# Kernel tuning notes

Hardware: AMD Instinct MI355X
Metric: run time of the kernel (lower is better)

Reference implementation:

```python
import jax, jax.numpy as jnp
import numpy as np

V, E, H, O, B, T = 50000, 128, 128, 128, 64, 512


def setup_inputs() -> dict:
    key = jax.random.key(0)
    ks = jax.random.split(key, 16)
    s = 0.05
    X = jax.random.randint(ks[0], (B, T), 0, V)
    lens = jnp.sort(jax.random.randint(ks[1], (B,), 64, T + 1))[::-1]
    lens = lens.at[0].set(T)  # pack_padded needs descending lengths, max == T
    emb = jax.random.normal(ks[2], (V, E)) * s
    emb = emb.at[0].set(0.0)  # padding_idx = 0
    return {
        "X": X,
        "X_lengths": lens,
        "batch_size": B,
        "emb": emb,
        "W_e2i": jax.random.normal(ks[3], (H, E)) * s,
        "b_e2i": jax.random.normal(ks[4], (H,)) * s,
        "Wih_f": jax.random.normal(ks[5], (3 * H, H)) * s,
        "Whh_f": jax.random.normal(ks[6], (3 * H, H)) * s,
        "bih_f": jax.random.normal(ks[7], (3 * H,)) * s,
        "bhh_f": jax.random.normal(ks[8], (3 * H,)) * s,
        "Wih_b": jax.random.normal(ks[9], (3 * H, H)) * s,
        "Whh_b": jax.random.normal(ks[10], (3 * H, H)) * s,
        "bih_b": jax.random.normal(ks[11], (3 * H,)) * s,
        "bhh_b": jax.random.normal(ks[12], (3 * H,)) * s,
        "W_h2o": jax.random.normal(ks[13], (O, 2 * H)) * s,
        "b_h2o": jax.random.normal(ks[14], (O,)) * s,
        "u_w": jax.random.uniform(ks[15], (O,)),  # torch.rand
    }


def _gru_scan(gx, mask_tb, Whh, bhh):
    """gx: [T,B,3H] precomputed input gates; mask_tb: [T,B,1] valid-step mask.
    Masked update emulates pack_padded_sequence: padded steps keep h unchanged
    (and h stays 0 before the first valid step of the reversed direction)."""
    h0 = jnp.zeros((gx.shape[1], Whh.shape[1]), gx.dtype)

    def step(h, tb):
        gxt, m = tb
        gh = h @ Whh.T + bhh
        gxr, gxz, gxn = jnp.split(gxt, 3, axis=-1)
        ghr, ghz, ghn = jnp.split(gh, 3, axis=-1)
        r = jax.nn.sigmoid(gxr + ghr)
        z = jax.nn.sigmoid(gxz + ghz)
        n = jnp.tanh(gxn + r * ghn)
        h_new = (1.0 - z) * n + z * h
        h = jnp.where(m, h_new, h)
        return h, h

    _, hs = jax.lax.scan(step, h0, (gx, mask_tb))
    return hs  # [T,B,H]


def reference(X, X_lengths, batch_size, emb, W_e2i, b_e2i,
              Wih_f, Whh_f, bih_f, bhh_f, Wih_b, Whh_b, bih_b, bhh_b,
              W_h2o, b_h2o, u_w):
    x = emb[X]                              # [B,T,E]
    x = x @ W_e2i.T + b_e2i                 # [B,T,H]
    Tn = x.shape[1]
    mask = jnp.arange(Tn)[None, :] < X_lengths[:, None]  # [B,T]
    m_tb = mask.T[:, :, None]               # [T,B,1]

    gx_f = (x @ Wih_f.T + bih_f).transpose(1, 0, 2)       # [T,B,3H]
    h_f = _gru_scan(gx_f, m_tb, Whh_f, bhh_f)             # [T,B,H]
    gx_b = (x @ Wih_b.T + bih_b).transpose(1, 0, 2)[::-1]
    h_b = _gru_scan(gx_b, m_tb[::-1], Whh_b, bhh_b)[::-1]

    Hout = jnp.concatenate([h_f, h_b], axis=-1).transpose(1, 0, 2)  # [B,T,2H]
    Hout = Hout * mask[:, :, None].astype(Hout.dtype)  # pad_packed zeros pads

    Y = jnp.tanh(Hout @ W_h2o.T + b_h2o)               # [B,T,O]
    scores = jnp.where(mask, (Y * u_w).sum(-1), -jnp.inf)  # [B,T]
    alpha = jax.nn.softmax(scores, axis=1)             # per-sample softmax over valid steps
    pooled = jnp.einsum("bt,btd->bd", alpha, Hout)     # [B,2H]
    return pooled[None]                                # [1,B,2H]
```

## Files before the change

### kernel.cpp

```cpp
#include <hip/hip_runtime.h>
#include <hip/hip_bf16.h>

#define VV 50000
#define EE 128
#define HH 128
#define OO 128
#define BB 64
#define TT 512

typedef __bf16 bf16_t;
typedef __attribute__((ext_vector_type(8))) __bf16 bf16x8;
typedef __attribute__((ext_vector_type(4))) __bf16 bf16x4;
typedef __attribute__((ext_vector_type(4))) float floatx4;

#define SC_RZ (-1.4426950408889634f)
#define SC_N  (2.8853900817779268f)

__device__ __forceinline__ bf16x8 ldb8(const bf16_t* p) {
    return *reinterpret_cast<const bf16x8*>(p);
}

__device__ __forceinline__ bf16x8 ldf8_bf(const float* p) {
    const float4* q = reinterpret_cast<const float4*>(p);
    float4 u = q[0], v = q[1];
    bf16x8 r;
    r[0] = (__bf16)u.x; r[1] = (__bf16)u.y; r[2] = (__bf16)u.z; r[3] = (__bf16)u.w;
    r[4] = (__bf16)v.x; r[5] = (__bf16)v.y; r[6] = (__bf16)v.z; r[7] = (__bf16)v.w;
    return r;
}

__device__ __forceinline__ float fast_rcp(float x) { return __builtin_amdgcn_rcpf(x); }
__device__ __forceinline__ float exp2_f(float x) { return __builtin_amdgcn_exp2f(x); }
__device__ __forceinline__ float tanh_f(float x) {
    float e = __expf(2.0f * x);
    return 1.0f - 2.0f * fast_rcp(e + 1.0f);
}

__device__ __forceinline__ void lds_barrier() {
    asm volatile("s_waitcnt lgkmcnt(0)\n\ts_barrier" ::: "memory");
}

__global__ __launch_bounds__(256) void k0_conv(
    const float* __restrict__ we,
    const float* __restrict__ wihf, const float* __restrict__ wihb,
    const float* __restrict__ whhf, const float* __restrict__ whhb,
    const float* __restrict__ wh2o,
    const float* __restrict__ bihf, const float* __restrict__ bhhf,
    const float* __restrict__ bihb, const float* __restrict__ bhhb,
    bf16_t* __restrict__ we_bf,
    bf16_t* __restrict__ wih_bf, bf16_t* __restrict__ whh_bf,
    bf16_t* __restrict__ wh2o_bf, float* __restrict__ gxbias) {
    int tid = blockIdx.x * 256 + threadIdx.x;
    int np = gridDim.x * 256;
    for (int i = tid; i < HH * EE; i += np) we_bf[i] = (bf16_t)we[i];
    for (int i = tid; i < 384 * HH; i += np) {
        int nrow = i >> 7;
        float sc = (nrow < 256) ? SC_RZ : SC_N;
        wih_bf[i] = (bf16_t)(sc * wihf[i]);
        wih_bf[384 * HH + i] = (bf16_t)(sc * wihb[i]);
        whh_bf[i] = (bf16_t)(sc * whhf[i]);
        whh_bf[384 * HH + i] = (bf16_t)(sc * whhb[i]);
    }
    for (int i = tid; i < OO * 256; i += np) wh2o_bf[i] = (bf16_t)wh2o[i];
    if (tid < 768) {
        int dir = tid / 384, n = tid % 384;
        const float* bih = dir ? bihb : bihf;
        const float* bhh = dir ? bhhb : bhhf;
        float sc = (n < 256) ? SC_RZ : SC_N;
        gxbias[tid] = sc * bih[n] + (n < 256 ? sc * bhh[n] : 0.0f);
    }
}

__global__ __launch_bounds__(256) void k12_gx(const int* __restrict__ X,
                                              const float* __restrict__ emb,
                                              const bf16_t* __restrict__ we_bf,
                                              const float* __restrict__ be,
                                              const bf16_t* __restrict__ wih_bf,
                                              const float* __restrict__ gxbias,
                                              const int* __restrict__ lens,
                                              bf16_t* __restrict__ gx3) {
    int blk = blockIdx.x;
    int tq = blk >> 2;
    int g = blk & 3;
    if (4 * tq >= lens[16 * g]) return;

    int lane = threadIdx.x & 63;
    int w2 = threadIdx.x >> 6;
    int quad = lane >> 4, col = lane & 15;

    __shared__ bf16_t xs[4][16 * 136];

    {
        int t = 4 * tq + w2;
        int v = X[(g * 16 + col) * TT + t];
        bf16x8 a[4];
#pragma unroll
        for (int kc = 0; kc < 4; ++kc)
            a[kc] = ldf8_bf(emb + (size_t)v * EE + kc * 32 + quad * 8);
#pragma unroll
        for (int nt = 0; nt < 8; ++nt) {
            int n = nt * 16 + col;
            floatx4 acc = {0.f, 0.f, 0.f, 0.f};
#pragma unroll
            for (int kc = 0; kc < 4; ++kc) {
                bf16x8 bw = ldb8(we_bf + (size_t)n * EE + kc * 32 + quad * 8);
                acc = __builtin_amdgcn_mfma_f32_16x16x32_bf16(a[kc], bw, acc, 0, 0, 0);
            }
            float bias = be[n];
#pragma unroll
            for (int r = 0; r < 4; ++r)
                xs[w2][(quad * 4 + r) * 136 + n] = (bf16_t)(acc[r] + bias);
        }
    }
    __syncthreads();

    bf16x8 a2[4][4];
#pragma unroll
    for (int tt = 0; tt < 4; ++tt)
#pragma unroll
        for (int kc = 0; kc < 4; ++kc)
            a2[tt][kc] = ldb8(xs[tt] + col * 136 + kc * 32 + quad * 8);

#pragma unroll 2
    for (int tl = 0; tl < 12; ++tl) {
        int idx = w2 * 12 + tl;
        int dir = idx >= 24;
        int n = (idx - dir * 24) * 16 + col;
        bf16x8 bw[4];
#pragma unroll
        for (int kc = 0; kc < 4; ++kc)
            bw[kc] = ldb8(wih_bf + ((size_t)dir * 384 + n) * HH + kc * 32 + quad * 8);
        float bias = gxbias[dir * 384 + n];
#pragma unroll
        for (int tt = 0; tt < 4; ++tt) {
            int t = 4 * tq + tt;
            floatx4 acc = {0.f, 0.f, 0.f, 0.f};
#pragma unroll
            for (int kc = 0; kc < 4; ++kc)
                acc = __builtin_amdgcn_mfma_f32_16x16x32_bf16(a2[tt][kc], bw[kc], acc, 0, 0, 0);
            bf16x4 pack;
#pragma unroll
            for (int r = 0; r < 4; ++r)
                pack[r] = (__bf16)(acc[r] + bias);
            *reinterpret_cast<bf16x4*>(
                gx3 + (((size_t)(dir * 16 + 4 * g + quad) * TT + t) * 384 + n) * 4) = pack;
        }
    }
}

#define HPAD 144
#define HBUF (4 * HPAD)
__global__ __launch_bounds__(512) void k3_gru(const bf16_t* __restrict__ gx3,
                                              const bf16_t* __restrict__ whh_bf,
                                              const float* __restrict__ bhh_f,
                                              const float* __restrict__ bhh_b,
                                              const int* __restrict__ lens,
                                              bf16_t* __restrict__ hist2) {
    int g16 = blockIdx.x;
    int dir = blockIdx.y;
    const float* bhh = dir ? bhh_b : bhh_f;

    int tid = threadIdx.x;
    int w = tid >> 6;
    int lane = tid & 63;
    int quad = lane >> 4, col = lane & 15;
    int j = 16 * w + col;

    __shared__ bf16_t hl[2 * HBUF];
    for (int i = tid; i < 2 * HBUF; i += 512) hl[i] = (bf16_t)0.f;

    int len1 = lens[4 * g16 + quad];
    int Lmax = max(max(lens[4 * g16], lens[4 * g16 + 1]),
                   max(lens[4 * g16 + 2], lens[4 * g16 + 3]));

    float bhn = SC_N * bhh[256 + j];

    bf16x8 Bw[3][4];
#pragma unroll
    for (int gate = 0; gate < 3; ++gate)
#pragma unroll
        for (int kc = 0; kc < 4; ++kc)
            Bw[gate][kc] = ldb8(whh_bf + ((size_t)dir * 384 + gate * 128 + j) * HH + kc * 32 + quad * 8);

    const bf16_t* gbase = gx3 + (size_t)(dir * 16 + g16) * TT * 1536;
    bf16_t* hb = hist2 + (size_t)(dir * 16 + g16) * TT * 512;
    int loff[3];
#pragma unroll
    for (int gate = 0; gate < 3; ++gate)
        loff[gate] = (gate * 128 + j) * 4 + quad;
    int hoff = quad * 128 + j;
    int aoff = (col >> 2) * HPAD + quad * 8;

    float h = 0.f;
    int S4 = (Lmax + 3) & ~3;

    __bf16 ring[4][3];
#pragma unroll
    for (int u = 0; u < 4; ++u) {
        int t = dir ? (Lmax - 1 - u) : u;
#pragma unroll
        for (int gate = 0; gate < 3; ++gate)
            ring[u][gate] = gbase[(size_t)t * 1536 + loff[gate]];
    }
    lds_barrier();

    int gstep = dir ? -1536 : 1536;
    int hstep = dir ? -512 : 512;
    const bf16_t* rp0 = gbase + (size_t)(dir ? (Lmax - 5) : 4) * 1536 + loff[0];
    const bf16_t* rp1 = gbase + (size_t)(dir ? (Lmax - 5) : 4) * 1536 + loff[1];
    const bf16_t* rp2 = gbase + (size_t)(dir ? (Lmax - 5) : 4) * 1536 + loff[2];
    bf16_t* hp = hb + (size_t)(dir ? (Lmax - 1) : 0) * 512 + hoff;
    int ulo = dir ? (Lmax - len1) : 0;
    int uhi = dir ? Lmax : len1;

    for (int sb = 0; sb < S4; sb += 4) {
#pragma unroll
        for (int u = 0; u < 4; ++u) {
            int s = sb + u;
            const bf16_t* hc = hl + (s & 1) * HBUF;
            bf16_t* hn = hl + ((s + 1) & 1) * HBUF;

            float gx0 = (float)ring[u][0];
            float gx1 = (float)ring[u][1];
            float gx2 = (float)ring[u][2];

            bf16x8 a[4];
#pragma unroll
            for (int kc = 0; kc < 4; ++kc)
                a[kc] = ldb8(hc + aoff + kc * 32);

            floatx4 cr = {0.f, 0.f, 0.f, 0.f};
            floatx4 cz = {0.f, 0.f, 0.f, 0.f};
            floatx4 cn = {bhn, bhn, bhn, bhn};
#pragma unroll
            for (int kc = 0; kc < 4; ++kc) {
                cr = __builtin_amdgcn_mfma_f32_16x16x32_bf16(a[kc], Bw[0][kc], cr, 0, 0, 0);
                cz = __builtin_amdgcn_mfma_f32_16x16x32_bf16(a[kc], Bw[1][kc], cz, 0, 0, 0);
                cn = __builtin_amdgcn_mfma_f32_16x16x32_bf16(a[kc], Bw[2][kc], cn, 0, 0, 0);
            }

            ring[u][0] = *rp0;
            ring[u][1] = *rp1;
            ring[u][2] = *rp2;
            {
                int adv = (s < Lmax - 5) ? gstep : 0;
                rp0 += adv; rp1 += adv; rp2 += adv;
            }

            float rg = fast_rcp(1.0f + exp2_f(cr[0] + gx0));
            float zg = fast_rcp(1.0f + exp2_f(cz[0] + gx1));
            float v  = fmaf(rg, cn[0], gx2);
            float ng = fmaf(-2.0f, fast_rcp(exp2_f(v) + 1.0f), 1.0f);
            float hnew = fmaf(zg, h - ng, ng);

            bool upd = (s >= ulo) && (s < uhi);
            h = upd ? hnew : h;
            bf16_t h16 = (bf16_t)h;
            hn[quad * HPAD + j] = h16;
            *hp = h16;
            hp += (s < Lmax - 1) ? hstep : 0;

            lds_barrier();
        }
    }
}

__global__ __launch_bounds__(512) void k45_pool(const bf16_t* __restrict__ hist2,
                                                const bf16_t* __restrict__ wh2o_bf,
                                                const float* __restrict__ bh2o,
                                                const float* __restrict__ uw,
                                                const int* __restrict__ lens,
                                                float* __restrict__ out) {
    int b = blockIdx.x;
    int g16 = b >> 2, bl = b & 3;
    int tid = threadIdx.x;
    int lane = tid & 63, wv = tid >> 6;
    int quad = lane >> 4, col = lane & 15;
    int len = lens[b];

    int p = wv >> 2;
    int q = wv & 3;

    __shared__ float smax[TT][4];
    __shared__ float alpha[TT];
    __shared__ float redw[16];
    __shared__ float red2[16 * 32 * 9];

    const bf16_t* hf = hist2 + (size_t)g16 * TT * 512 + bl * 128;
    const bf16_t* hbk = hist2 + (size_t)(16 + g16) * TT * 512 + bl * 128;

    int n0 = (q * 2 + 0) * 16 + col;
    int n1 = (q * 2 + 1) * 16 + col;
    float bias0 = bh2o[n0], u0 = uw[n0];
    float bias1 = bh2o[n1], u1 = uw[n1];

    bf16x8 bw0[8], bw1[8];
#pragma unroll
    for (int kc = 0; kc < 8; ++kc) {
        bw0[kc] = ldb8(wh2o_bf + (size_t)n0 * 256 + kc * 32 + quad * 8);
        bw1[kc] = ldb8(wh2o_bf + (size_t)n1 * 256 + kc * 32 + quad * 8);
    }

    int nch = (len + 15) >> 4;
    bf16x8 a[8], an[8];
    {
        int t = p * 16 + col;
#pragma unroll
        for (int kc = 0; kc < 4; ++kc) {
            a[kc]     = ldb8(hf  + (size_t)t * 512 + kc * 32 + quad * 8);
            a[kc + 4] = ldb8(hbk + (size_t)t * 512 + kc * 32 + quad * 8);
        }
    }
    for (int ch = p; ch < nch; ch += 2) {
        int t0 = ch * 16;
        {
            int tn = (ch + 2 < nch ? t0 + 32 : t0) + col;
#pragma unroll
            for (int kc = 0; kc < 4; ++kc) {
                an[kc]     = ldb8(hf  + (size_t)tn * 512 + kc * 32 + quad * 8);
                an[kc + 4] = ldb8(hbk + (size_t)tn * 512 + kc * 32 + quad * 8);
            }
        }
        float p4[4] = {0.f, 0.f, 0.f, 0.f};
#pragma unroll
        for (int tl = 0; tl < 2; ++tl) {
            float bias = tl ? bias1 : bias0;
            float u = tl ? u1 : u0;
            floatx4 accA = {0.f, 0.f, 0.f, 0.f};
            floatx4 accB = {0.f, 0.f, 0.f, 0.f};
#pragma unroll
            for (int kc = 0; kc < 4; ++kc) {
                bf16x8 bwA = tl ? bw1[kc] : bw0[kc];
                bf16x8 bwB = tl ? bw1[kc + 4] : bw0[kc + 4];
                accA = __builtin_amdgcn_mfma_f32_16x16x32_bf16(a[kc], bwA, accA, 0, 0, 0);
                accB = __builtin_amdgcn_mfma_f32_16x16x32_bf16(a[kc + 4], bwB, accB, 0, 0, 0);
            }
#pragma unroll
            for (int r = 0; r < 4; ++r)
                p4[r] += tanh_f(accA[r] + accB[r] + bias) * u;
        }
#pragma unroll
        for (int m = 1; m < 16; m <<= 1)
#pragma unroll
            for (int r = 0; r < 4; ++r)
                p4[r] += __shfl_xor(p4[r], m, 64);
        if (col == 0) {
#pragma unroll
            for (int r = 0; r < 4; ++r)
                smax[t0 + quad * 4 + r][q] = p4[r];
        }
#pragma unroll
        for (int kc = 0; kc < 8; ++kc) a[kc] = an[kc];
    }
    __syncthreads();

    int t = tid;
    float s = -1e30f;
    if (t < len) s = smax[t][0] + smax[t][1] + smax[t][2] + smax[t][3];
    float m = s;
#pragma unroll
    for (int off = 1; off <= 32; off <<= 1) m = fmaxf(m, __shfl_xor(m, off, 64));
    if (lane == 0) redw[wv] = m;
    __syncthreads();
    float mx = fmaxf(fmaxf(fmaxf(redw[0], redw[1]), fmaxf(redw[2], redw[3])),
                     fmaxf(fmaxf(redw[4], redw[5]), fmaxf(redw[6], redw[7])));
    float e = (t < len) ? __expf(s - mx) : 0.f;
    alpha[t] = e;
    float sm = e;
#pragma unroll
    for (int off = 1; off <= 32; off <<= 1) sm += __shfl_xor(sm, off, 64);
    if (lane == 0) redw[8 + wv] = sm;
    __syncthreads();
    float inv = fast_rcp(redw[8] + redw[9] + redw[10] + redw[11] +
                         redw[12] + redw[13] + redw[14] + redw[15]);

    {
        int ts = tid >> 5, o = tid & 31;
        int dirp = o >> 4;
        int j8 = (o & 15) * 8;
        const bf16_t* hbase = (dirp ? hbk : hf) + j8;
        float acc8[8];
#pragma unroll
        for (int ee = 0; ee < 8; ++ee) acc8[ee] = 0.f;
        for (int tt2 = ts; tt2 < len; tt2 += 16) {
            float al = alpha[tt2];
            bf16x8 hv = ldb8(hbase + (size_t)tt2 * 512);
#pragma unroll
            for (int ee = 0; ee < 8; ++ee) acc8[ee] = fmaf(al, (float)hv[ee], acc8[ee]);
        }
#pragma unroll
        for (int ee = 0; ee < 8; ++ee) red2[(ts * 32 + o) * 9 + ee] = acc8[ee];
        __syncthreads();
        if (tid < 256) {
            int c = tid;
            int dir2 = c >> 7, rem = c & 127;
            int oo = dir2 * 16 + (rem >> 3), ee = c & 7;
            float acc = 0.f;
#pragma unroll
            for (int qq = 0; qq < 16; ++qq) acc += red2[(qq * 32 + oo) * 9 + ee];
            out[(size_t)b * 256 + c] = acc * inv;
        }
    }
}

extern "C" void kernel_launch(void* const* d_in, const int* in_sizes, int n_in,
                              void* d_out, int out_size, void* d_ws, size_t ws_size,
                              hipStream_t stream) {
    const int* X       = (const int*)d_in[0];
    const int* lens    = (const int*)d_in[1];
    const float* emb   = (const float*)d_in[3];
    const float* We2i  = (const float*)d_in[4];
    const float* be2i  = (const float*)d_in[5];
    const float* Wihf  = (const float*)d_in[6];
    const float* Whhf  = (const float*)d_in[7];
    const float* bihf  = (const float*)d_in[8];
    const float* bhhf  = (const float*)d_in[9];
    const float* Wihb  = (const float*)d_in[10];
    const float* Whhb  = (const float*)d_in[11];
    const float* bihb  = (const float*)d_in[12];
    const float* bhhb  = (const float*)d_in[13];
    const float* Wh2o  = (const float*)d_in[14];
    const float* bh2o  = (const float*)d_in[15];
    const float* uw    = (const float*)d_in[16];

    char* ws = (char*)d_ws;
    size_t off = 0;
    bf16_t* we_bf = (bf16_t*)(ws + off);   off += (size_t)HH * EE * 2;
    bf16_t* wih_bf = (bf16_t*)(ws + off);  off += (size_t)2 * 384 * HH * 2;
    bf16_t* whh_bf = (bf16_t*)(ws + off);  off += (size_t)2 * 384 * HH * 2;
    bf16_t* wh2o_bf = (bf16_t*)(ws + off); off += (size_t)OO * 256 * 2;
    float* gxbias = (float*)(ws + off);    off += 768 * 4;
    off = (off + 255) & ~(size_t)255;
    bf16_t* gx3 = (bf16_t*)(ws + off);     off += (size_t)32 * TT * 384 * 4 * 2;
    bf16_t* hist2 = (bf16_t*)(ws + off);   off += (size_t)32 * TT * 4 * 128 * 2;

    float* out = (float*)d_out;

    k0_conv<<<dim3(256), dim3(256), 0, stream>>>(We2i, Wihf, Wihb, Whhf, Whhb,
                                                 Wh2o, bihf, bhhf, bihb, bhhb,
                                                 we_bf, wih_bf, whh_bf, wh2o_bf, gxbias);
    k12_gx<<<dim3(TT), dim3(256), 0, stream>>>(X, emb, we_bf, be2i, wih_bf, gxbias, lens, gx3);
    k3_gru<<<dim3(16, 2), dim3(512), 0, stream>>>(gx3, whh_bf, bhhf, bhhb, lens, hist2);
    k45_pool<<<dim3(BB), dim3(512), 0, stream>>>(hist2, wh2o_bf, bh2o, uw, lens, out);
}
```

Baseline: 341.7 us.

## Split score and pooling kernels to spread attention scoring over more blocks

Splits the fused score/pool kernel in two. The scoring MFMA work is now spread across four blocks per sample (256 blocks instead of 64), and partial scores go to a global workspace. A second kernel per sample reads the scores, runs the softmax and does the weighted pooling. This raises parallelism on the GPU's many CUs, at the cost of an extra launch and a global round trip for the scores.

```diff
diff --git a/kernel.cpp b/kernel.cpp
--- a/kernel.cpp
+++ b/kernel.cpp
@@ -265,13 +265,14 @@
     }
 }
 
-__global__ __launch_bounds__(512) void k45_pool(const bf16_t* __restrict__ hist2,
+__global__ __launch_bounds__(512) void k4_score(const bf16_t* __restrict__ hist2,
                                                 const bf16_t* __restrict__ wh2o_bf,
                                                 const float* __restrict__ bh2o,
                                                 const float* __restrict__ uw,
                                                 const int* __restrict__ lens,
-                                                float* __restrict__ out) {
-    int b = blockIdx.x;
+                                                float* __restrict__ smax_ws) {
+    int blk = blockIdx.x;
+    int b = blk >> 2, seg = blk & 3;
     int g16 = b >> 2, bl = b & 3;
     int tid = threadIdx.x;
     int lane = tid & 63, wv = tid >> 6;
@@ -280,14 +281,12 @@
 
     int p = wv >> 2;
     int q = wv & 3;
-
-    __shared__ float smax[TT][4];
-    __shared__ float alpha[TT];
-    __shared__ float redw[16];
-    __shared__ float red2[16 * 32 * 9];
+    int ch0 = seg * 2 + p;
+    int nch = (len + 15) >> 4;
 
     const bf16_t* hf = hist2 + (size_t)g16 * TT * 512 + bl * 128;
     const bf16_t* hbk = hist2 + (size_t)(16 + g16) * TT * 512 + bl * 128;
+    float* sm = smax_ws + (size_t)b * TT * 4;
 
     int n0 = (q * 2 + 0) * 16 + col;
     int n1 = (q * 2 + 1) * 16 + col;
@@ -301,20 +300,19 @@
         bw1[kc] = ldb8(wh2o_bf + (size_t)n1 * 256 + kc * 32 + quad * 8);
     }
 
-    int nch = (len + 15) >> 4;
     bf16x8 a[8], an[8];
     {
-        int t = p * 16 + col;
+        int t = ch0 * 16 + col;
 #pragma unroll
         for (int kc = 0; kc < 4; ++kc) {
             a[kc]     = ldb8(hf  + (size_t)t * 512 + kc * 32 + quad * 8);
             a[kc + 4] = ldb8(hbk + (size_t)t * 512 + kc * 32 + quad * 8);
         }
     }
-    for (int ch = p; ch < nch; ch += 2) {
+    for (int ch = ch0; ch < nch; ch += 8) {
         int t0 = ch * 16;
         {
-            int tn = (ch + 2 < nch ? t0 + 32 : t0) + col;
+            int tn = (ch + 8 < nch ? t0 + 128 : t0) + col;
 #pragma unroll
             for (int kc = 0; kc < 4; ++kc) {
                 an[kc]     = ldb8(hf  + (size_t)tn * 512 + kc * 32 + quad * 8);
@@ -347,16 +345,37 @@
         if (col == 0) {
 #pragma unroll
             for (int r = 0; r < 4; ++r)
-                smax[t0 + quad * 4 + r][q] = p4[r];
+                sm[(size_t)(t0 + quad * 4 + r) * 4 + q] = p4[r];
         }
 #pragma unroll
         for (int kc = 0; kc < 8; ++kc) a[kc] = an[kc];
     }
-    __syncthreads();
+}
+
+__global__ __launch_bounds__(512) void k5_pool(const bf16_t* __restrict__ hist2,
+                                               const float* __restrict__ smax_ws,
+                                               const int* __restrict__ lens,
+                                               float* __restrict__ out) {
+    int b = blockIdx.x;
+    int g16 = b >> 2, bl = b & 3;
+    int tid = threadIdx.x;
+    int lane = tid & 63, wv = tid >> 6;
+    int len = lens[b];
+
+    __shared__ float alpha[TT];
+    __shared__ float redw[16];
+    __shared__ float red2[16 * 32 * 9];
+
+    const bf16_t* hf = hist2 + (size_t)g16 * TT * 512 + bl * 128;
+    const bf16_t* hbk = hist2 + (size_t)(16 + g16) * TT * 512 + bl * 128;
+    const float* sm = smax_ws + (size_t)b * TT * 4;
 
     int t = tid;
     float s = -1e30f;
-    if (t < len) s = smax[t][0] + smax[t][1] + smax[t][2] + smax[t][3];
+    if (t < len) {
+        float4 v = *reinterpret_cast<const float4*>(sm + (size_t)t * 4);
+        s = (v.x + v.y) + (v.z + v.w);
+    }
     float m = s;
 #pragma unroll
     for (int off = 1; off <= 32; off <<= 1) m = fmaxf(m, __shfl_xor(m, off, 64));
@@ -366,10 +385,10 @@
                      fmaxf(fmaxf(redw[4], redw[5]), fmaxf(redw[6], redw[7])));
     float e = (t < len) ? __expf(s - mx) : 0.f;
     alpha[t] = e;
-    float sm = e;
-#pragma unroll
-    for (int off = 1; off <= 32; off <<= 1) sm += __shfl_xor(sm, off, 64);
-    if (lane == 0) redw[8 + wv] = sm;
+    float smm = e;
+#pragma unroll
+    for (int off = 1; off <= 32; off <<= 1) smm += __shfl_xor(smm, off, 64);
+    if (lane == 0) redw[8 + wv] = smm;
     __syncthreads();
     float inv = fast_rcp(redw[8] + redw[9] + redw[10] + redw[11] +
                          redw[12] + redw[13] + redw[14] + redw[15]);
@@ -431,6 +450,8 @@
     bf16_t* wh2o_bf = (bf16_t*)(ws + off); off += (size_t)OO * 256 * 2;
     float* gxbias = (float*)(ws + off);    off += 768 * 4;
     off = (off + 255) & ~(size_t)255;
+    float* smax_ws = (float*)(ws + off);   off += (size_t)BB * TT * 4 * 4;
+    off = (off + 255) & ~(size_t)255;
     bf16_t* gx3 = (bf16_t*)(ws + off);     off += (size_t)32 * TT * 384 * 4 * 2;
     bf16_t* hist2 = (bf16_t*)(ws + off);   off += (size_t)32 * TT * 4 * 128 * 2;
 
@@ -441,5 +462,6 @@
                                                  we_bf, wih_bf, whh_bf, wh2o_bf, gxbias);
     k12_gx<<<dim3(TT), dim3(256), 0, stream>>>(X, emb, we_bf, be2i, wih_bf, gxbias, lens, gx3);
     k3_gru<<<dim3(16, 2), dim3(512), 0, stream>>>(gx3, whh_bf, bhhf, bhhb, lens, hist2);
-    k45_pool<<<dim3(BB), dim3(512), 0, stream>>>(hist2, wh2o_bf, bh2o, uw, lens, out);
-}
+    k4_score<<<dim3(BB * 4), dim3(512), 0, stream>>>(hist2, wh2o_bf, bh2o, uw, lens, smax_ws);
+    k5_pool<<<dim3(BB), dim3(512), 0, stream>>>(hist2, smax_ws, lens, out);
+}
```

Result: faster. 327.1 us, median of 2 (-4.3%).
